# Kernel tuning notes

Measured on AMD Instinct MI355X. Metric: run time of the kernel, lower is better.

## Reference

```python
import jax, jax.numpy as jnp
import numpy as np

EPS = 1e-5

def _ln(x, g, b):
    mu = jnp.mean(x, axis=-1, keepdims=True)
    var = jnp.var(x, axis=-1, keepdims=True)
    return (x - mu) * jax.lax.rsqrt(var + EPS) * g + b

def setup_inputs() -> dict:
    key = jax.random.key(0)
    ks = jax.random.split(key, 8)
    B, L, D, H = 2, 2048, 1024, 16
    F = 4096
    s = 0.02
    return {
        "x": jax.random.normal(ks[0], (B, L, D), dtype=jnp.float32),
        "attn_mask": jnp.tril(jnp.ones((L, L), dtype=jnp.float32)),
        # weights stored [in, out] (equivalent to torch Linear weight.T)
        "w_qkuv": jax.random.normal(ks[1], (D, 4 * D), dtype=jnp.float32) * s,
        "w_out": jax.random.normal(ks[2], (D, D), dtype=jnp.float32) * s,
        "w1": jax.random.normal(ks[3], (D, F), dtype=jnp.float32) * s,
        "w2": jax.random.normal(ks[4], (F, D), dtype=jnp.float32) * s,
        "w3": jax.random.normal(ks[5], (D, F), dtype=jnp.float32) * s,
        "ln1_g": jnp.ones((D,), jnp.float32), "ln1_b": jnp.zeros((D,), jnp.float32),
        "ln2_g": jnp.ones((D,), jnp.float32), "ln2_b": jnp.zeros((D,), jnp.float32),
        "na_g": jnp.ones((D // H,), jnp.float32), "na_b": jnp.zeros((D // H,), jnp.float32),
    }

def reference(x, attn_mask, w_qkuv, w_out, w1, w2, w3,
              ln1_g, ln1_b, ln2_g, ln2_b, na_g, na_b):
    B, L, D = x.shape
    H = 16
    d = D // H
    # --- SiLU attention sublayer ---
    xn = _ln(x, ln1_g, ln1_b)
    qkuv = jax.nn.silu(xn @ w_qkuv)                       # [B, L, 4D]
    q, k, v, u = jnp.split(qkuv, 4, axis=-1)
    def heads(t):
        return t.reshape(B, L, H, d).transpose(0, 2, 1, 3)  # [B, H, L, d]
    q, k, v, u = heads(q), heads(k), heads(v), heads(u)
    scores = jnp.einsum('bhqd,bhkd->bhqk', q, k) / jnp.sqrt(jnp.float32(d))
    scores = jax.nn.silu(scores) * attn_mask              # broadcast [L, L] over B, H
    a = jnp.einsum('bhqk,bhkd->bhqd', scores, v)          # [B, H, L, d]
    a = _ln(a, na_g, na_b) * u
    a = a.transpose(0, 2, 1, 3).reshape(B, L, D)
    x = x + a @ w_out
    # --- SwiGLU FFN sublayer ---
    xn2 = _ln(x, ln2_g, ln2_b)
    x = x + (jax.nn.silu(xn2 @ w1) * (xn2 @ w3)) @ w2
    return x
```

## Files before the change

kernel.cpp:

```cpp
#include <hip/hip_runtime.h>
#include <hip/hip_bf16.h>

typedef __hip_bfloat16 bf16;
typedef __attribute__((ext_vector_type(8))) short short8;
typedef __attribute__((ext_vector_type(4))) short bfv4;
typedef __attribute__((ext_vector_type(4))) float f32x4;
typedef __attribute__((ext_vector_type(4))) unsigned short us4;

#define LN_EPS 1e-5f

__device__ __forceinline__ float siluf(float x) { return x / (1.f + __expf(-x)); }
__device__ __forceinline__ unsigned short f2bf_bits(float f) {
    bf16 h = __float2bfloat16(f);
    return *reinterpret_cast<unsigned short*>(&h);
}
__device__ __forceinline__ bf16 f2bf(float f) { return __float2bfloat16(f); }
__device__ __forceinline__ float bf2f(bf16 h) { return __bfloat162float(h); }

__device__ __forceinline__ void load_lds16(const void* g, void* l) {
    __builtin_amdgcn_global_load_lds((const __attribute__((address_space(1))) void*)g,
                                     (__attribute__((address_space(3))) void*)l, 16, 0, 0);
}

__device__ __forceinline__ f32x4 mfma16(bfv4 a, bfv4 b, f32x4 c) {
    return __builtin_amdgcn_mfma_f32_16x16x16bf16_1k(a, b, c, 0, 0, 0);
}

__device__ __forceinline__ void drain_and_sync() {
    asm volatile("s_waitcnt vmcnt(0)" ::: "memory");
    __builtin_amdgcn_sched_barrier(0);
    __syncthreads();
}

template <int N>
__device__ __forceinline__ void wait_vmcnt() {
    asm volatile("s_waitcnt vmcnt(%0)" :: "n"(N) : "memory");
}
__device__ __forceinline__ void hard_barrier() {
    __builtin_amdgcn_sched_barrier(0);
    __builtin_amdgcn_s_barrier();
    __builtin_amdgcn_sched_barrier(0);
}
__device__ __forceinline__ void lgkm_barrier() {
    asm volatile("s_waitcnt lgkmcnt(0)" ::: "memory");
    __builtin_amdgcn_sched_barrier(0);
    __builtin_amdgcn_s_barrier();
    __builtin_amdgcn_sched_barrier(0);
}

__device__ __forceinline__ void phase_pre() {
    __builtin_amdgcn_sched_barrier(0);
    __builtin_amdgcn_s_barrier();
    asm volatile("s_waitcnt lgkmcnt(0)" ::: "memory");
    __builtin_amdgcn_sched_barrier(0);
    __builtin_amdgcn_s_setprio(1);
}
__device__ __forceinline__ void phase_post() {
    __builtin_amdgcn_s_setprio(0);
    __builtin_amdgcn_sched_barrier(0);
    __builtin_amdgcn_s_barrier();
    __builtin_amdgcn_sched_barrier(0);
}

__device__ __forceinline__ int xcd_swz(int bid, int nwg) {
    return (bid & 7) * (nwg >> 3) + (bid >> 3);
}

__global__ __launch_bounds__(256) void transpose_cast(
    const float* __restrict__ src, bf16* __restrict__ dst, int K, int N)
{
    __shared__ float t[32][33];
    const int nb = blockIdx.x << 5, kb = blockIdx.y << 5;
    const int tx = threadIdx.x, ty = threadIdx.y;
#pragma unroll
    for (int i = ty; i < 32; i += 8) t[i][tx] = src[(size_t)(kb + i) * N + nb + tx];
    __syncthreads();
#pragma unroll
    for (int i = ty; i < 32; i += 8) dst[(size_t)(nb + i) * K + kb + tx] = f2bf(t[tx][i]);
}

__global__ __launch_bounds__(256) void transpose_cast3(
    const float* __restrict__ s0, const float* __restrict__ s1, const float* __restrict__ s2,
    bf16* __restrict__ d0, bf16* __restrict__ d1, bf16* __restrict__ d2)
{
    const float* src = (blockIdx.z == 0) ? s0 : (blockIdx.z == 1) ? s1 : s2;
    bf16* dst = (blockIdx.z == 0) ? d0 : (blockIdx.z == 1) ? d1 : d2;
    const int K = 1024, N = 4096;
    __shared__ float t[32][33];
    const int nb = blockIdx.x << 5, kb = blockIdx.y << 5;
    const int tx = threadIdx.x, ty = threadIdx.y;
#pragma unroll
    for (int i = ty; i < 32; i += 8) t[i][tx] = src[(size_t)(kb + i) * N + nb + tx];
    __syncthreads();
#pragma unroll
    for (int i = ty; i < 32; i += 8) dst[(size_t)(nb + i) * K + kb + tx] = f2bf(t[tx][i]);
}

__global__ __launch_bounds__(256) void ln_cast(
    const float* __restrict__ x, const float* __restrict__ g, const float* __restrict__ be,
    bf16* __restrict__ out)
{
    const int row = blockIdx.x, tid = threadIdx.x;
    const float4 v = ((const float4*)(x + (size_t)row * 1024))[tid];
    float s = v.x + v.y + v.z + v.w;
    float ss = v.x * v.x + v.y * v.y + v.z * v.z + v.w * v.w;
#pragma unroll
    for (int o = 32; o; o >>= 1) { s += __shfl_down(s, o); ss += __shfl_down(ss, o); }
    __shared__ float red[10];
    const int wid = tid >> 6, lane = tid & 63;
    if (lane == 0) { red[wid] = s; red[4 + wid] = ss; }
    __syncthreads();
    if (tid == 0) {
        float S = red[0] + red[1] + red[2] + red[3];
        float SS = red[4] + red[5] + red[6] + red[7];
        float mu = S * (1.f / 1024.f);
        red[8] = mu;
        red[9] = rsqrtf(SS * (1.f / 1024.f) - mu * mu + LN_EPS);
    }
    __syncthreads();
    const float mu = red[8], rstd = red[9];
    const float4 gg = ((const float4*)g)[tid];
    const float4 bb = ((const float4*)be)[tid];
    us4 o;
    o[0] = f2bf_bits((v.x - mu) * rstd * gg.x + bb.x);
    o[1] = f2bf_bits((v.y - mu) * rstd * gg.y + bb.y);
    o[2] = f2bf_bits((v.z - mu) * rstd * gg.z + bb.z);
    o[3] = f2bf_bits((v.w - mu) * rstd * gg.w + bb.w);
    ((us4*)(out + (size_t)row * 1024))[tid] = o;
}

template <int EPI>
__global__ __launch_bounds__(512, 2) void gemm8(
    const bf16* __restrict__ A, const bf16* __restrict__ BT,
    bf16* __restrict__ outp, const bf16* __restrict__ mulsrc,
    int M, int N, int K)
{
    __shared__ __align__(16) bf16 lds[2][2][256 * 64];
    const int tid = threadIdx.x;
    const int wid = tid >> 6, lane = tid & 63;
    const int lhi = lane >> 4, llo = lane & 15;
    const int nby = M >> 8;
    const int bid = xcd_swz((int)blockIdx.x, (int)gridDim.x);
    const int by = bid % nby, bx = bid / nby;
    const int row0 = by << 8, col0 = bx << 8;
    const int wr = wid >> 2, wc = wid & 3;
    const int wbase = wid << 6;

    auto stage_tile = [&](const bf16* src, int r0, int k0, char* ldsbase) {
#pragma unroll
        for (int it = 0; it < 4; ++it) {
            const int p = it * 512 + wbase + lane;
            const int r = p >> 3, pc = p & 7;
            const int lc = pc ^ (r & 7);
            load_lds16(src + (size_t)(r0 + r) * K + k0 + lc * 8,
                       ldsbase + (size_t)(it * 512 + wbase) * 16);
        }
    };
    auto stageA = [&](int t) { stage_tile(A, row0, t << 6, (char*)lds[t & 1][0]); };
    auto stageB = [&](int t) { stage_tile(BT, col0, t << 6, (char*)lds[t & 1][1]); };

    f32x4 acc[8][4] = {};

    stageA(0); stageB(0);
    wait_vmcnt<0>();
    hard_barrier();

    const int KT = K >> 6;
    for (int t = 0; t < KT; ++t) {
        const bool more = (t + 1 < KT);
        const char* lAc = (const char*)lds[t & 1][0];
        const char* lBc = (const char*)lds[t & 1][1];

        short8 a0[2][4], a1[2][4], b0[2][2], b1[2][2];
        auto ldA = [&](short8 af[2][4], int mh) {
#pragma unroll
            for (int kk = 0; kk < 2; ++kk)
#pragma unroll
                for (int m = 0; m < 4; ++m) {
                    const int ra = wr * 128 + mh * 64 + m * 16 + llo;
                    af[kk][m] = *(const short8*)(lAc + ra * 128 + (((kk * 4 + lhi) ^ (ra & 7)) << 4));
                }
        };
        auto ldB = [&](short8 bf_[2][2], int nh) {
#pragma unroll
            for (int kk = 0; kk < 2; ++kk)
#pragma unroll
                for (int n = 0; n < 2; ++n) {
                    const int rb = wc * 64 + nh * 32 + n * 16 + llo;
                    bf_[kk][n] = *(const short8*)(lBc + rb * 128 + (((kk * 4 + lhi) ^ (rb & 7)) << 4));
                }
        };
        auto mfma_q = [&](int mh, int nh, short8 af[2][4], short8 bf_[2][2]) {
#pragma unroll
            for (int kk = 0; kk < 2; ++kk)
#pragma unroll
                for (int m = 0; m < 4; ++m)
#pragma unroll
                    for (int n = 0; n < 2; ++n)
                        acc[mh * 4 + m][nh * 2 + n] =
                            __builtin_amdgcn_mfma_f32_16x16x32_bf16(af[kk][m], bf_[kk][n], acc[mh * 4 + m][nh * 2 + n], 0, 0, 0);
        };

        ldA(a0, 0); ldB(b0, 0);
        if (more) stageA(t + 1);
        phase_pre(); mfma_q(0, 0, a0, b0); phase_post();
        ldB(b1, 1);
        if (more) stageB(t + 1);
        phase_pre(); mfma_q(0, 1, a0, b1); phase_post();
        ldA(a1, 1);
        phase_pre(); mfma_q(1, 1, a1, b1); phase_post();
        phase_pre(); mfma_q(1, 0, a1, b0); phase_post();

        if (more) { wait_vmcnt<0>(); hard_barrier(); }
    }

#pragma unroll
    for (int m = 0; m < 8; ++m) {
        const int rbase = row0 + wr * 128 + m * 16 + lhi * 4;
#pragma unroll
        for (int n = 0; n < 4; ++n) {
            const int c = col0 + wc * 64 + n * 16 + llo;
#pragma unroll
            for (int r = 0; r < 4; ++r) {
                const size_t idx = (size_t)(rbase + r) * N + c;
                const float v = acc[m][n][r];
                if constexpr (EPI == 0) outp[idx] = f2bf(siluf(v));
                else                    outp[idx] = f2bf(v * bf2f(mulsrc[idx]));
            }
        }
    }
}

__global__ __launch_bounds__(512, 2) void gemm_w13_8(
    const bf16* __restrict__ A, const bf16* __restrict__ B1T, const bf16* __restrict__ B3T,
    bf16* __restrict__ outp, int M, int N, int K)
{
    __shared__ __align__(16) bf16 lA[2][256 * 64];
    __shared__ __align__(16) bf16 lB1[2][128 * 64];
    __shared__ __align__(16) bf16 lB3[2][128 * 64];
    const int tid = threadIdx.x;
    const int wid = tid >> 6, lane = tid & 63;
    const int lhi = lane >> 4, llo = lane & 15;
    const int nby = M >> 8;
    const int bid = xcd_swz((int)blockIdx.x, (int)gridDim.x);
    const int by = bid % nby, bx = bid / nby;
    const int row0 = by << 8, col0 = bx << 7;
    const int wr = wid >> 2, wc = wid & 3;
    const int wbase = wid << 6;

    auto stage_rows = [&](const bf16* src, int r0, int k0, char* ldsbase, int nit) {
        for (int it = 0; it < nit; ++it) {
            const int p = it * 512 + wbase + lane;
            const int r = p >> 3, pc = p & 7;
            const int lc = pc ^ (r & 7);
            load_lds16(src + (size_t)(r0 + r) * K + k0 + lc * 8,
                       ldsbase + (size_t)(it * 512 + wbase) * 16);
        }
    };
    auto stageA = [&](int t) { stage_rows(A, row0, t << 6, (char*)lA[t & 1], 4); };
    auto stageB = [&](int t) {
        stage_rows(B1T, col0, t << 6, (char*)lB1[t & 1], 2);
        stage_rows(B3T, col0, t << 6, (char*)lB3[t & 1], 2);
    };

    f32x4 acc1[8][2] = {}, acc3[8][2] = {};

    stageA(0); stageB(0);
    wait_vmcnt<0>();
    hard_barrier();

    const int KT = K >> 6;
    for (int t = 0; t < KT; ++t) {
        const bool more = (t + 1 < KT);
        const char* lAc = (const char*)lA[t & 1];
        const char* lB1c = (const char*)lB1[t & 1];
        const char* lB3c = (const char*)lB3[t & 1];

        short8 b1f[2], b3f[2];
        auto ldA4 = [&](short8 af[4], int mh, int kk) {
#pragma unroll
            for (int m = 0; m < 4; ++m) {
                const int ra = wr * 128 + mh * 64 + m * 16 + llo;
                af[m] = *(const short8*)(lAc + ra * 128 + (((kk * 4 + lhi) ^ (ra & 7)) << 4));
            }
        };
        auto ldBk = [&](int kk) {
#pragma unroll
            for (int n = 0; n < 2; ++n) {
                const int rb = wc * 32 + n * 16 + llo;
                const int so = (((kk * 4 + lhi) ^ (rb & 7)) << 4);
                b1f[n] = *(const short8*)(lB1c + rb * 128 + so);
                b3f[n] = *(const short8*)(lB3c + rb * 128 + so);
            }
        };
        auto mfma_p = [&](short8 af[4], int mh) {
#pragma unroll
            for (int m = 0; m < 4; ++m)
#pragma unroll
                for (int n = 0; n < 2; ++n) {
                    acc1[mh * 4 + m][n] = __builtin_amdgcn_mfma_f32_16x16x32_bf16(af[m], b1f[n], acc1[mh * 4 + m][n], 0, 0, 0);
                    acc3[mh * 4 + m][n] = __builtin_amdgcn_mfma_f32_16x16x32_bf16(af[m], b3f[n], acc3[mh * 4 + m][n], 0, 0, 0);
                }
        };

        short8 af[4];
        ldA4(af, 0, 0); ldBk(0);
        if (more) stageA(t + 1);
        phase_pre(); mfma_p(af, 0); phase_post();
        ldA4(af, 1, 0);
        if (more) stageB(t + 1);
        phase_pre(); mfma_p(af, 1); phase_post();
        ldA4(af, 0, 1); ldBk(1);
        phase_pre(); mfma_p(af, 0); phase_post();
        ldA4(af, 1, 1);
        phase_pre(); mfma_p(af, 1); phase_post();

        if (more) { wait_vmcnt<0>(); hard_barrier(); }
    }

#pragma unroll
    for (int m = 0; m < 8; ++m) {
        const int rbase = row0 + wr * 128 + m * 16 + lhi * 4;
#pragma unroll
        for (int n = 0; n < 2; ++n) {
            const int c = col0 + wc * 32 + n * 16 + llo;
#pragma unroll
            for (int r = 0; r < 4; ++r) {
                const size_t idx = (size_t)(rbase + r) * N + c;
                outp[idx] = f2bf(siluf(acc1[m][n][r]) * acc3[m][n][r]);
            }
        }
    }
}

__global__ __launch_bounds__(256) void gemm_btc(
    const bf16* __restrict__ A, const bf16* __restrict__ BT,
    float* __restrict__ outp, const float* __restrict__ resid,
    int M, int N, int K)
{
    __shared__ __align__(16) bf16 lA[2][128 * 64];
    __shared__ __align__(16) bf16 lB[2][64 * 64];
    const int tid = threadIdx.x;
    const int wid = tid >> 6, lane = tid & 63;
    const int lhi = lane >> 4, llo = lane & 15;
    const int ntx = N >> 6;
    const int bid = xcd_swz((int)blockIdx.x, (int)gridDim.x);
    const int bx = bid % ntx, by = bid / ntx;
    const int row0 = by << 7, col0 = bx << 6;
    const int wr = wid >> 1, wc = wid & 1;
    const int wbase = wid << 6;

    auto stage_tile = [&](const bf16* src, int r0, int k0, char* ldsbase, int nit) {
        for (int it = 0; it < nit; ++it) {
            const int p = it * 256 + wbase + lane;
            const int r = p >> 3, pc = p & 7;
            const int lc = pc ^ (r & 7);
            load_lds16(src + (size_t)(r0 + r) * K + k0 + lc * 8,
                       ldsbase + (size_t)(it * 256 + wbase) * 16);
        }
    };
    auto stageT = [&](int t) {
        stage_tile(A, row0, t << 6, (char*)lA[t & 1], 4);
        stage_tile(BT, col0, t << 6, (char*)lB[t & 1], 2);
    };

    f32x4 acc[4][2] = {};

    stageT(0); stageT(1);
    wait_vmcnt<6>();
    hard_barrier();

    const int KT = K >> 6;
    for (int t = 0; t < KT; ++t) {
        const int buf = t & 1;
        const char* lAc = (const char*)lA[buf];
        const char* lBc = (const char*)lB[buf];

        short8 af[4], bfr[2];
        auto ldA = [&](int kk) {
#pragma unroll
            for (int m = 0; m < 4; ++m) {
                const int ra = wr * 64 + m * 16 + llo;
                af[m] = *(const short8*)(lAc + ra * 128 + (((kk * 4 + lhi) ^ (ra & 7)) << 4));
            }
        };
        auto ldB = [&](int kk) {
#pragma unroll
            for (int n = 0; n < 2; ++n) {
                const int rb = wc * 32 + n * 16 + llo;
                bfr[n] = *(const short8*)(lBc + rb * 128 + (((kk * 4 + lhi) ^ (rb & 7)) << 4));
            }
        };

#pragma unroll
        for (int kk = 0; kk < 2; ++kk) {
            ldA(kk); ldB(kk);
            __builtin_amdgcn_s_setprio(1);
#pragma unroll
            for (int m = 0; m < 4; ++m)
#pragma unroll
                for (int n = 0; n < 2; ++n)
                    acc[m][n] = __builtin_amdgcn_mfma_f32_16x16x32_bf16(af[m], bfr[n], acc[m][n], 0, 0, 0);
            __builtin_amdgcn_s_setprio(0);
        }

        lgkm_barrier();
        if (t + 2 < KT) {
            stageT(t + 2);
            wait_vmcnt<6>();
            hard_barrier();
        } else if (t + 1 < KT) {
            wait_vmcnt<0>();
            hard_barrier();
        }
    }

#pragma unroll
    for (int m = 0; m < 4; ++m) {
        const int rbase = row0 + wr * 64 + m * 16 + lhi * 4;
#pragma unroll
        for (int n = 0; n < 2; ++n) {
            const int c = col0 + wc * 32 + n * 16 + llo;
#pragma unroll
            for (int r = 0; r < 4; ++r) {
                const size_t idx = (size_t)(rbase + r) * N + c;
                outp[idx] = resid[idx] + acc[m][n][r];
            }
        }
    }
}

__global__ __launch_bounds__(256) void v_trans(const bf16* __restrict__ qkuv, bf16* __restrict__ v_t)
{
    __shared__ bf16 t[64][65];
    const int bh = blockIdx.y;
    const int b = bh >> 4, h = bh & 15;
    const int l0 = blockIdx.x << 6;
    const int tx = threadIdx.x, ty = threadIdx.y;
#pragma unroll
    for (int i = ty; i < 64; i += 4)
        t[i][tx] = qkuv[(size_t)(b * 2048 + l0 + i) * 4096 + 2048 + h * 64 + tx];
    __syncthreads();
#pragma unroll
    for (int i = ty; i < 64; i += 4)
        v_t[(size_t)(bh * 64 + i) * 2048 + l0 + tx] = t[tx][i];
}

__global__ __launch_bounds__(512) void attn_kernel(
    const bf16* __restrict__ qkuv, const bf16* __restrict__ v_t,
    const float* __restrict__ nag, const float* __restrict__ nab,
    bf16* __restrict__ au)
{
    __shared__ __align__(16) bf16 lK[2][128 * 64];
    __shared__ __align__(16) bf16 lV[2][64 * 128];
    const int tid = threadIdx.x;
    const int wid = tid >> 6, lane = tid & 63;
    const int lhi = lane >> 4, llo = lane & 15;
    const int bid = (int)blockIdx.x;
    const int qt = 15 - (bid >> 5);
    const int bh = bid & 31;
    const int b = bh >> 4, h = bh & 15;
    const int q0 = qt << 7;
    const bf16* Qb = qkuv + (size_t)b * 2048 * 4096 + h * 64;
    const bf16* Kb = Qb + 1024;
    const bf16* Ub = Qb + 3072;
    const bf16* Vb = v_t + (size_t)bh * 64 * 2048;
    const int wbase = wid << 6;

    auto stage = [&](int kt_s, int buf) {
        const int koff = kt_s << 7;
        char* lKc = (char*)lK[buf];
        char* lVc = (char*)lV[buf];
#pragma unroll
        for (int it = 0; it < 2; ++it) {
            const int p = it * 512 + wbase + lane;
            const int r = p >> 3, pc = p & 7;
            const int lc = pc ^ (r & 7);
            load_lds16(Kb + (size_t)(koff + r) * 4096 + lc * 8, lKc + (it * 512 + wbase) * 16);
        }
#pragma unroll
        for (int it = 0; it < 2; ++it) {
            const int p = it * 512 + wbase + lane;
            const int d = p >> 4, pc = p & 15;
            const int lc = pc ^ (d & 15);
            load_lds16(Vb + (size_t)d * 2048 + koff + lc * 8, lVc + (it * 512 + wbase) * 16);
        }
    };

    short8 qb[2];
#pragma unroll
    for (int kk = 0; kk < 2; ++kk)
        qb[kk] = *(const short8*)(Qb + (size_t)(q0 + wid * 16 + llo) * 4096 + kk * 32 + lhi * 8);

    f32x4 acc2[4] = {};

    stage(0, 0);

    for (int kt = 0; kt <= qt; ++kt) {
        const int cur = kt & 1;
        drain_and_sync();
        if (kt < qt) stage(kt + 1, cur ^ 1);
        const char* lKc = (const char*)lK[cur];
        const char* lVc = (const char*)lV[cur];

        const bool diag = (kt == qt);
#pragma unroll
        for (int m = 0; m < 8; ++m) {
            if (diag && m > wid) break;
            const int rK = m * 16 + llo;
            const int sw = rK & 7;
            short8 ak0 = *(const short8*)(lKc + rK * 128 + ((lhi ^ sw) << 4));
            short8 ak1 = *(const short8*)(lKc + rK * 128 + (((4 + lhi) ^ sw) << 4));
            f32x4 s = {};
            s = __builtin_amdgcn_mfma_f32_16x16x32_bf16(ak0, qb[0], s, 0, 0, 0);
            s = __builtin_amdgcn_mfma_f32_16x16x32_bf16(ak1, qb[1], s, 0, 0, 0);
            const bool mask = diag && (m == wid);
            bfv4 a16;
#pragma unroll
            for (int r = 0; r < 4; ++r) {
                float xx = s[r] * 0.125f;
                xx = xx * __builtin_amdgcn_rcpf(1.f + __expf(-xx));
                if (mask && (lhi * 4 + r > llo)) xx = 0.f;
                a16[r] = (short)f2bf_bits(xx);
            }
#pragma unroll
            for (int dcol = 0; dcol < 4; ++dcol) {
                const int d = dcol * 16 + llo;
                const int lcV = m * 2 + (lhi >> 1);
                bfv4 bv = *(const bfv4*)(lVc + d * 256 + ((lcV ^ llo) << 4) + (lhi & 1) * 8);
                acc2[dcol] = mfma16(a16, bv, acc2[dcol]);
            }
        }
    }

#pragma unroll
    for (int r = 0; r < 4; ++r) {
        float vv[4];
        float s = 0.f, ss = 0.f;
#pragma unroll
        for (int dc = 0; dc < 4; ++dc) { vv[dc] = acc2[dc][r]; s += vv[dc]; ss += vv[dc] * vv[dc]; }
#pragma unroll
        for (int o = 1; o < 16; o <<= 1) { s += __shfl_xor(s, o); ss += __shfl_xor(ss, o); }
        const float mu = s * (1.f / 64.f);
        const float rstd = rsqrtf(ss * (1.f / 64.f) - mu * mu + LN_EPS);
        const int q = wid * 16 + lhi * 4 + r;
        const size_t grow = q0 + q;
#pragma unroll
        for (int dc = 0; dc < 4; ++dc) {
            const int c = dc * 16 + llo;
            const float nv = (vv[dc] - mu) * rstd * nag[c] + nab[c];
            const float uu = bf2f(Ub[grow * 4096 + c]);
            au[(size_t)(b * 2048 + grow) * 1024 + h * 64 + c] = f2bf(nv * uu);
        }
    }
}

extern "C" void kernel_launch(void* const* d_in, const int* in_sizes, int n_in,
                              void* d_out, int out_size, void* d_ws, size_t ws_size,
                              hipStream_t stream)
{
    const float* x      = (const float*)d_in[0];
    const float* w_qkuv = (const float*)d_in[2];
    const float* w_out  = (const float*)d_in[3];
    const float* w1     = (const float*)d_in[4];
    const float* w2     = (const float*)d_in[5];
    const float* w3     = (const float*)d_in[6];
    const float* ln1g   = (const float*)d_in[7];
    const float* ln1b   = (const float*)d_in[8];
    const float* ln2g   = (const float*)d_in[9];
    const float* ln2b   = (const float*)d_in[10];
    const float* nag    = (const float*)d_in[11];
    const float* nab    = (const float*)d_in[12];
    float* out = (float*)d_out;

    char* ws = (char*)d_ws;
    size_t off = 0;
    auto alloc = [&](size_t bytes) { void* p = ws + off; off += (bytes + 255) & ~(size_t)255; return p; };
    const size_t M = 4096;
    bf16* wqkuvT = (bf16*)alloc(4096ull * 1024 * 2);
    bf16* woutT  = (bf16*)alloc(1024ull * 1024 * 2);
    bf16* w1T    = (bf16*)alloc(4096ull * 1024 * 2);
    bf16* w3T    = (bf16*)alloc(4096ull * 1024 * 2);
    bf16* w2T    = (bf16*)alloc(1024ull * 4096 * 2);
    bf16* xn     = (bf16*)alloc(M * 1024 * 2);
    bf16* qkuv   = (bf16*)alloc(M * 4096 * 2);
    bf16* vt     = (bf16*)alloc(32ull * 64 * 2048 * 2);
    bf16* aub    = (bf16*)alloc(M * 1024 * 2);
    float* x2    = (float*)alloc(M * 1024 * 4);
    bf16* xn2    = (bf16*)alloc(M * 1024 * 2);
    bf16* h1     = (bf16*)alloc(M * 4096 * 2);
    (void)ws_size; (void)in_sizes; (void)n_in; (void)out_size;

    dim3 tb(32, 8);
    transpose_cast3<<<dim3(4096 / 32, 1024 / 32, 3), tb, 0, stream>>>(w_qkuv, w1, w3, wqkuvT, w1T, w3T);
    transpose_cast<<<dim3(1024 / 32, 1024 / 32), tb, 0, stream>>>(w_out, woutT, 1024, 1024);
    transpose_cast<<<dim3(1024 / 32, 4096 / 32), tb, 0, stream>>>(w2, w2T, 4096, 1024);

    ln_cast<<<M, 256, 0, stream>>>(x, ln1g, ln1b, xn);

    gemm8<0><<<dim3((M / 256) * (4096 / 256)), 512, 0, stream>>>(xn, wqkuvT, qkuv, nullptr, M, 4096, 1024);

    v_trans<<<dim3(2048 / 64, 32), dim3(64, 4), 0, stream>>>(qkuv, vt);

    attn_kernel<<<dim3(512), 512, 0, stream>>>(qkuv, vt, nag, nab, aub);

    gemm_btc<<<dim3((M / 128) * (1024 / 64)), 256, 0, stream>>>(aub, woutT, x2, x, M, 1024, 1024);

    ln_cast<<<M, 256, 0, stream>>>(x2, ln2g, ln2b, xn2);

    gemm_w13_8<<<dim3((M / 256) * (4096 / 128)), 512, 0, stream>>>(xn2, w1T, w3T, h1, M, 4096, 1024);

    gemm_btc<<<dim3((M / 128) * (1024 / 64)), 256, 0, stream>>>(h1, w2T, out, x2, M, 1024, 4096);
}
```

Before: 280.4 us.

## Shrink fused W1/W3 GEMM tile to 128x128 with K-step of 32

The fused SwiGLU W1/W3 GEMM moves from a 256x128 block tile with K-step 64 to a 128x128 tile with K-step 32. The LDS layout and swizzle are reworked to pack two rows per 128-byte line, and each thread now issues one global-to-LDS load per matrix per step. The goal is a much smaller LDS footprint and fewer accumulator registers, doubling the grid for more occupancy and parallelism. The cost is lower arithmetic intensity per block, twice as many K iterations and barriers, and more repeated global traffic for the B operands.

After: 284.2 us. About the same (+1.4%).

```diff
diff --git a/kernel.cpp b/kernel.cpp
--- a/kernel.cpp
+++ b/kernel.cpp
@@ -231,96 +231,93 @@
     }
 }
 
-__global__ __launch_bounds__(512, 2) void gemm_w13_8(
+__global__ __launch_bounds__(512) void gemm_w13_8(
     const bf16* __restrict__ A, const bf16* __restrict__ B1T, const bf16* __restrict__ B3T,
     bf16* __restrict__ outp, int M, int N, int K)
 {
-    __shared__ __align__(16) bf16 lA[2][256 * 64];
-    __shared__ __align__(16) bf16 lB1[2][128 * 64];
-    __shared__ __align__(16) bf16 lB3[2][128 * 64];
+    __shared__ __align__(16) bf16 lA[2][64 * 64];
+    __shared__ __align__(16) bf16 lB1[2][64 * 64];
+    __shared__ __align__(16) bf16 lB3[2][64 * 64];
     const int tid = threadIdx.x;
     const int wid = tid >> 6, lane = tid & 63;
     const int lhi = lane >> 4, llo = lane & 15;
-    const int nby = M >> 8;
+    const int nby = M >> 7;
     const int bid = xcd_swz((int)blockIdx.x, (int)gridDim.x);
     const int by = bid % nby, bx = bid / nby;
-    const int row0 = by << 8, col0 = bx << 7;
+    const int row0 = by << 7, col0 = bx << 7;
     const int wr = wid >> 2, wc = wid & 3;
     const int wbase = wid << 6;
 
-    auto stage_rows = [&](const bf16* src, int r0, int k0, char* ldsbase, int nit) {
-        for (int it = 0; it < nit; ++it) {
-            const int p = it * 512 + wbase + lane;
-            const int r = p >> 3, pc = p & 7;
-            const int lc = pc ^ (r & 7);
-            load_lds16(src + (size_t)(r0 + r) * K + k0 + lc * 8,
-                       ldsbase + (size_t)(it * 512 + wbase) * 16);
-        }
+    auto stage_rows = [&](const bf16* src, int r0, int k0, char* ldsbase) {
+        const int p = wbase + lane;
+        const int pr = p >> 3, pc = p & 7;
+        const int r = pr * 2 + (pc >> 2);
+        const int lc = (pc & 3) ^ (pr & 3);
+        load_lds16(src + (size_t)(r0 + r) * K + k0 + lc * 8, ldsbase + p * 16);
     };
-    auto stageA = [&](int t) { stage_rows(A, row0, t << 6, (char*)lA[t & 1], 4); };
-    auto stageB = [&](int t) {
-        stage_rows(B1T, col0, t << 6, (char*)lB1[t & 1], 2);
-        stage_rows(B3T, col0, t << 6, (char*)lB3[t & 1], 2);
+    auto stageT = [&](int t) {
+        const int k0 = t << 5, buf = t & 1;
+        stage_rows(A, row0, k0, (char*)lA[buf]);
+        stage_rows(B1T, col0, k0, (char*)lB1[buf]);
+        stage_rows(B3T, col0, k0, (char*)lB3[buf]);
     };
-
-    f32x4 acc1[8][2] = {}, acc3[8][2] = {};
-
-    stageA(0); stageB(0);
+    auto rdaddr = [&](int r, int kc) {
+        return (r >> 1) * 128 + (r & 1) * 64 + ((kc ^ ((r >> 1) & 3)) << 4);
+    };
+
+    f32x4 acc1[4][2] = {}, acc3[4][2] = {};
+
+    stageT(0);
     wait_vmcnt<0>();
     hard_barrier();
 
-    const int KT = K >> 6;
+    const int KT = K >> 5;
     for (int t = 0; t < KT; ++t) {
         const bool more = (t + 1 < KT);
         const char* lAc = (const char*)lA[t & 1];
         const char* lB1c = (const char*)lB1[t & 1];
         const char* lB3c = (const char*)lB3[t & 1];
 
-        short8 b1f[2], b3f[2];
-        auto ldA4 = [&](short8 af[4], int mh, int kk) {
-#pragma unroll
-            for (int m = 0; m < 4; ++m) {
-                const int ra = wr * 128 + mh * 64 + m * 16 + llo;
-                af[m] = *(const short8*)(lAc + ra * 128 + (((kk * 4 + lhi) ^ (ra & 7)) << 4));
-            }
-        };
-        auto ldBk = [&](int kk) {
+        short8 af[4], b1f[2], b3f[2];
+#pragma unroll
+        for (int m = 0; m < 4; ++m) {
+            const int ra = wr * 64 + m * 16 + llo;
+            af[m] = *(const short8*)(lAc + rdaddr(ra, lhi));
+        }
+#pragma unroll
+        for (int n = 0; n < 2; ++n) {
+            const int rb = wc * 32 + n * 16 + llo;
+            const int so = rdaddr(rb, lhi);
+            b1f[n] = *(const short8*)(lB1c + so);
+            b3f[n] = *(const short8*)(lB3c + so);
+        }
+        if (more) stageT(t + 1);
+
+        phase_pre();
+#pragma unroll
+        for (int m = 0; m < 2; ++m)
 #pragma unroll
             for (int n = 0; n < 2; ++n) {
-                const int rb = wc * 32 + n * 16 + llo;
-                const int so = (((kk * 4 + lhi) ^ (rb & 7)) << 4);
-                b1f[n] = *(const short8*)(lB1c + rb * 128 + so);
-                b3f[n] = *(const short8*)(lB3c + rb * 128 + so);
-            }
-        };
-        auto mfma_p = [&](short8 af[4], int mh) {
-#pragma unroll
-            for (int m = 0; m < 4; ++m)
-#pragma unroll
-                for (int n = 0; n < 2; ++n) {
-                    acc1[mh * 4 + m][n] = __builtin_amdgcn_mfma_f32_16x16x32_bf16(af[m], b1f[n], acc1[mh * 4 + m][n], 0, 0, 0);
-                    acc3[mh * 4 + m][n] = __builtin_amdgcn_mfma_f32_16x16x32_bf16(af[m], b3f[n], acc3[mh * 4 + m][n], 0, 0, 0);
-                }
-        };
-
-        short8 af[4];
-        ldA4(af, 0, 0); ldBk(0);
-        if (more) stageA(t + 1);
-        phase_pre(); mfma_p(af, 0); phase_post();
-        ldA4(af, 1, 0);
-        if (more) stageB(t + 1);
-        phase_pre(); mfma_p(af, 1); phase_post();
-        ldA4(af, 0, 1); ldBk(1);
-        phase_pre(); mfma_p(af, 0); phase_post();
-        ldA4(af, 1, 1);
-        phase_pre(); mfma_p(af, 1); phase_post();
+                acc1[m][n] = __builtin_amdgcn_mfma_f32_16x16x32_bf16(af[m], b1f[n], acc1[m][n], 0, 0, 0);
+                acc3[m][n] = __builtin_amdgcn_mfma_f32_16x16x32_bf16(af[m], b3f[n], acc3[m][n], 0, 0, 0);
+            }
+        phase_post();
+        phase_pre();
+#pragma unroll
+        for (int m = 2; m < 4; ++m)
+#pragma unroll
+            for (int n = 0; n < 2; ++n) {
+                acc1[m][n] = __builtin_amdgcn_mfma_f32_16x16x32_bf16(af[m], b1f[n], acc1[m][n], 0, 0, 0);
+                acc3[m][n] = __builtin_amdgcn_mfma_f32_16x16x32_bf16(af[m], b3f[n], acc3[m][n], 0, 0, 0);
+            }
+        phase_post();
 
         if (more) { wait_vmcnt<0>(); hard_barrier(); }
     }
 
 #pragma unroll
-    for (int m = 0; m < 8; ++m) {
-        const int rbase = row0 + wr * 128 + m * 16 + lhi * 4;
+    for (int m = 0; m < 4; ++m) {
+        const int rbase = row0 + wr * 64 + m * 16 + lhi * 4;
 #pragma unroll
         for (int n = 0; n < 2; ++n) {
             const int c = col0 + wc * 32 + n * 16 + llo;
@@ -608,7 +605,7 @@
 
     ln_cast<<<M, 256, 0, stream>>>(x2, ln2g, ln2b, xn2);
 
-    gemm_w13_8<<<dim3((M / 256) * (4096 / 128)), 512, 0, stream>>>(xn2, w1T, w3T, h1, M, 4096, 1024);
+    gemm_w13_8<<<dim3((M / 128) * (4096 / 128)), 512, 0, stream>>>(xn2, w1T, w3T, h1, M, 4096, 1024);
 
     gemm_btc<<<dim3((M / 128) * (1024 / 64)), 256, 0, stream>>>(h1, w2T, out, x2, M, 1024, 4096);
 }
```
